# Performance work log

Hardware: AMD Instinct MI355X
Metric: run time of the kernel (lower is better)

## Reference

```python
import jax, jax.numpy as jnp
import numpy as np

B, S, HID = 1, 2048, 2048
H, KV, D = 32, 8, 64          # query heads, kv heads, head_dim
N_REP = H // KV
BASE = 10000.0


def rotate_half(x):
    x1, x2 = x[..., : D // 2], x[..., D // 2 :]
    return jnp.concatenate((-x2, x1), axis=-1)


def setup_inputs() -> dict:
    key = jax.random.key(0)
    ks = jax.random.split(key, 6)
    std = 0.02
    return {
        "hidden_states": jax.random.normal(ks[0], (B, S, HID), jnp.float32),
        "position_ids": jnp.broadcast_to(jnp.arange(S, dtype=jnp.int32), (B, S)),
        "powers": jax.random.normal(ks[1], (D // 2,), jnp.float32),
        "Wq": jax.random.normal(ks[2], (H * D, HID), jnp.float32) * std,
        "Wk": jax.random.normal(ks[3], (KV * D, HID), jnp.float32) * std,
        "Wv": jax.random.normal(ks[4], (KV * D, HID), jnp.float32) * std,
        "Wo": jax.random.normal(ks[5], (HID, H * D), jnp.float32) * std,
    }


def reference(hidden_states, position_ids, powers, Wq, Wk, Wv, Wo):
    bsz, q_len, _ = hidden_states.shape

    # QKV projections (no bias)
    q = (hidden_states @ Wq.T).reshape(bsz, q_len, H, D).transpose(0, 2, 1, 3)   # [B,H,S,D]
    k = (hidden_states @ Wk.T).reshape(bsz, q_len, KV, D).transpose(0, 2, 1, 3)  # [B,KV,S,D]
    v = (hidden_states @ Wv.T).reshape(bsz, q_len, KV, D).transpose(0, 2, 1, 3)

    # Learnable RoPE: inv_freq = base ** (-sigmoid(powers))
    inv_freq = 1.0 / (BASE ** jax.nn.sigmoid(powers))                 # [D/2]
    freqs = position_ids.astype(jnp.float32)[:, :, None] * inv_freq  # [B,S,D/2]
    emb = jnp.concatenate((freqs, freqs), axis=-1)                   # [B,S,D]
    cos = jnp.cos(emb)[:, None, :, :]                                # [B,1,S,D]
    sin = jnp.sin(emb)[:, None, :, :]

    q = q * cos + rotate_half(q) * sin
    k = k * cos + rotate_half(k) * sin

    # GQA: repeat_interleave kv heads
    k = jnp.repeat(k, N_REP, axis=1)  # [B,H,S,D]
    v = jnp.repeat(v, N_REP, axis=1)

    scores = jnp.einsum("bhqd,bhkd->bhqk", q, k) / np.sqrt(D).astype(np.float32)
    # additive causal mask (module is_causal=True)
    pos = jnp.arange(q_len)
    causal = jnp.where(pos[:, None] >= pos[None, :], 0.0, jnp.finfo(jnp.float32).min)
    scores = scores + causal

    probs = jax.nn.softmax(scores.astype(jnp.float32), axis=-1).astype(q.dtype)
    attn = jnp.einsum("bhqk,bhkd->bhqd", probs, v)                   # [B,H,S,D]
    attn = attn.transpose(0, 2, 1, 3).reshape(bsz, q_len, H * D)
    return attn @ Wo.T
```

## Files before the change

kernel.cpp:

```cpp
#include <hip/hip_runtime.h>

typedef unsigned short u16;
typedef __attribute__((ext_vector_type(8))) short short8;
typedef __attribute__((ext_vector_type(4))) short s16x4;
typedef __attribute__((ext_vector_type(4))) float f32x4;
typedef __attribute__((ext_vector_type(16))) float f32x16;
typedef __attribute__((ext_vector_type(4))) unsigned u32x4;

#define S_LEN 2048
#define HID 2048
#define NQH 32
#define NKV 8
#define HD 64
#define QKVN 3072
#define SCLOG2 0.1803368801111204f

__device__ __forceinline__ short f2b(float f){
  unsigned u = __builtin_bit_cast(unsigned, f);
  u += 0x7fffu + ((u >> 16) & 1u);
  return (short)(u >> 16);
}
__device__ __forceinline__ float b2f(u16 v){
  unsigned u = ((unsigned)v) << 16;
  return __builtin_bit_cast(float, u);
}
__device__ __forceinline__ void gll16(const void* g, void* l){
  __builtin_amdgcn_global_load_lds((const __attribute__((address_space(1))) void*)g,
                                   (__attribute__((address_space(3))) void*)l, 16, 0, 0);
}
__device__ __forceinline__ unsigned cvtpk(float a, float b){
  unsigned r;
  asm("v_cvt_pk_bf16_f32 %0, %1, %2" : "=v"(r) : "v"(a), "v"(b));
  return r;
}
__device__ __forceinline__ void pswap(unsigned &a, unsigned &b){
  asm volatile("v_permlane32_swap_b32 %0, %1" : "+v"(a), "+v"(b));
}
__device__ __forceinline__ float ex2(float x){
  float r; asm("v_exp_f32 %0, %1" : "=v"(r) : "v"(x)); return r;
}

__global__ __launch_bounds__(256) void cvt_all(const float* __restrict__ s0,
                                               const float* __restrict__ s1,
                                               const float* __restrict__ s2,
                                               const float* __restrict__ s3,
                                               const float* __restrict__ s4,
                                               u16* __restrict__ d0, u16* __restrict__ d1,
                                               u16* __restrict__ d2, u16* __restrict__ d3,
                                               u16* __restrict__ d4,
                                               const int* __restrict__ pos,
                                               const float* __restrict__ powers,
                                               float* __restrict__ cost,
                                               float* __restrict__ sint){
  int i = blockIdx.x * 256 + threadIdx.x;
  if (i >= 1835008) {
    int j = i - 1835008;
    int s = j >> 5, d = j & 31;
    float p = (float)pos[s];
    float w = powers[d];
    float sig = 1.0f / (1.0f + expf(-w));
    float inv = powf(10000.0f, -sig);
    float f = p * inv;
    cost[j] = cosf(f);
    sint[j] = sinf(f);
    return;
  }
  const float* s; u16* d; int off;
  if      (i <  524288){ s = s0; d = d0; off = i; }
  else if (i < 1048576){ s = s1; d = d1; off = i -  524288; }
  else if (i < 1179648){ s = s2; d = d2; off = i - 1048576; }
  else if (i < 1310720){ s = s3; d = d3; off = i - 1179648; }
  else                 { s = s4; d = d4; off = i - 1310720; }
  const float4* s4p = (const float4*)s;
  float4 a = s4p[off*2], b = s4p[off*2+1];
  short8 o = { f2b(a.x), f2b(a.y), f2b(a.z), f2b(a.w),
               f2b(b.x), f2b(b.y), f2b(b.z), f2b(b.w) };
  *(short8*)(d + (size_t)off*8) = o;
}

template<int MODE>
__global__ __launch_bounds__(256) void gemm_bt(const u16* __restrict__ A,
                                               const u16* __restrict__ B0,
                                               const u16* __restrict__ B1,
                                               const u16* __restrict__ B2,
                                               int n1, int n2,
                                               void* __restrict__ Cout,
                                               u16* __restrict__ vtOut,
                                               int M, int Ntot, int K,
                                               const float* __restrict__ cost,
                                               const float* __restrict__ sint){
  __shared__ alignas(16) u16 sA[2][64*64];
  __shared__ alignas(16) u16 sB[2][128*64];
  const int tid = threadIdx.x, lane = tid & 63, wv = tid >> 6;
  const int wr = wv >> 1, wc = wv & 1;
  const int m0 = blockIdx.y * 64, n0 = blockIdx.x * 128;
  const int lr = lane & 15, lg = lane >> 4;

  const u16* B;
  if (n0 < n1)      B = B0 + (size_t)n0 * K;
  else if (n0 < n2) B = B1 + (size_t)(n0 - n1) * K;
  else              B = B2 + (size_t)(n0 - n2) * K;

  const int sRow = tid >> 3;
  const int sCol = ((tid & 7) ^ (sRow & 7)) * 8;
  const u16* Arow = A + (size_t)(m0 + sRow)*K + sCol;
  const u16* Brow = B + (size_t)sRow*K + sCol;

  f32x4 acc[2][4] = {};
  const int NT = K >> 6;

  #pragma unroll
  for (int i = 0; i < 2; ++i)
    gll16(Arow + (size_t)i*32*K, (char*)&sA[0][0] + i*4096 + tid*16);
  #pragma unroll
  for (int i = 0; i < 4; ++i)
    gll16(Brow + (size_t)i*32*K, (char*)&sB[0][0] + i*4096 + tid*16);
  __syncthreads();

  for (int t = 0; t < NT; ++t) {
    const int cur = t & 1;
    if (t + 1 < NT) {
      const int kn = (t + 1) << 6;
      #pragma unroll
      for (int i = 0; i < 2; ++i)
        gll16(Arow + (size_t)i*32*K + kn, (char*)&sA[cur^1][0] + i*4096 + tid*16);
      #pragma unroll
      for (int i = 0; i < 4; ++i)
        gll16(Brow + (size_t)i*32*K + kn, (char*)&sB[cur^1][0] + i*4096 + tid*16);
    }
    const char* bA = (const char*)&sA[cur][0];
    const char* bB = (const char*)&sB[cur][0];
    #pragma unroll
    for (int kk = 0; kk < 64; kk += 32) {
      short8 af[2], bfr[4];
      #pragma unroll
      for (int m = 0; m < 2; ++m)
        af[m] = *(const short8*)(bA + (wr*32 + m*16 + lr)*128 + ((((kk>>3) + lg) ^ (lr & 7)) << 4));
      #pragma unroll
      for (int n = 0; n < 4; ++n)
        bfr[n] = *(const short8*)(bB + (wc*64 + n*16 + lr)*128 + ((((kk>>3) + lg) ^ (lr & 7)) << 4));
      #pragma unroll
      for (int m = 0; m < 2; ++m)
        #pragma unroll
        for (int n = 0; n < 4; ++n)
          acc[m][n] = __builtin_amdgcn_mfma_f32_16x16x32_bf16(af[m], bfr[n], acc[m][n], 0, 0, 0);
    }
    asm volatile("s_waitcnt vmcnt(0)" ::: "memory");
    __builtin_amdgcn_s_barrier();
  }

  if (MODE == 0 && n0 >= 2560) {
    #pragma unroll
    for (int n = 0; n < 4; ++n) {
      const int colv = n0 - 2560 + wc*64 + n*16 + lr;
      #pragma unroll
      for (int m = 0; m < 2; ++m) {
        const int row = m0 + wr*32 + m*16 + lg*4;
        s16x4 o = { f2b(acc[m][n][0]), f2b(acc[m][n][1]),
                    f2b(acc[m][n][2]), f2b(acc[m][n][3]) };
        *(s16x4*)&vtOut[(size_t)colv*S_LEN + row] = o;
      }
    }
  } else if (MODE == 0) {
    const float qsc = (n0 < n1) ? SCLOG2 : 1.0f;
    #pragma unroll
    for (int m = 0; m < 2; ++m)
      #pragma unroll
      for (int r = 0; r < 4; ++r) {
        int row = m0 + wr*32 + m*16 + lg*4 + r;
        float c0 = cost[row*32 + lr],      s0 = sint[row*32 + lr];
        float c1 = cost[row*32 + 16 + lr], s1 = sint[row*32 + 16 + lr];
        float x0 = acc[m][0][r], x1 = acc[m][1][r];
        float x2 = acc[m][2][r], x3 = acc[m][3][r];
        float o0 = (x0*c0 - x2*s0)*qsc, o2 = (x2*c0 + x0*s0)*qsc;
        float o1 = (x1*c1 - x3*s1)*qsc, o3 = (x3*c1 + x1*s1)*qsc;
        u16* cp = (u16*)Cout + (size_t)row*Ntot + n0 + wc*64 + lr;
        cp[0]  = (u16)f2b(o0);
        cp[16] = (u16)f2b(o1);
        cp[32] = (u16)f2b(o2);
        cp[48] = (u16)f2b(o3);
      }
  } else {
    #pragma unroll
    for (int m = 0; m < 2; ++m)
      #pragma unroll
      for (int n = 0; n < 4; ++n)
        #pragma unroll
        for (int r = 0; r < 4; ++r) {
          int row = m0 + wr*32 + m*16 + lg*4 + r;
          int col = n0 + wc*64 + n*16 + lr;
          ((float*)Cout)[(size_t)row*Ntot + col] = acc[m][n][r];
        }
  }
}

__global__ __launch_bounds__(256) void flash_attn(const u16* __restrict__ qkv,
                                                  const u16* __restrict__ vt,
                                                  u16* __restrict__ attn,
                                                  float* __restrict__ pO,
                                                  float* __restrict__ pL){
  __shared__ alignas(16) u16 sK[4][32*64];
  __shared__ alignas(16) u16 sVT[4][64*32];
  static const int c_tab[24] = {7,15,15,14,14,6,13,13,12,12,5,11,11,
                                10,10,4,9,9,8,8,3,2,1,0};
  static const int s_tab[24] = {2,0,1,0,1,2,0,1,0,1,2,0,1,
                                0,1,2,0,1,0,1,2,2,2,2};
  const int tid = threadIdx.x, lane = tid & 63, w = tid >> 6;
  const int h = blockIdx.x, kvh = h >> 2;
  const int chunk = c_tab[blockIdx.y];
  const int sl = s_tab[blockIdx.y];
  int t0, ntb;
  if (sl == 2) { t0 = 0; ntb = 4*chunk + 4; }
  else         { t0 = sl*2*(chunk + 1); ntb = 2*(chunk + 1); }

  const int l5 = lane & 31, hi = lane >> 5;
  const int q0w = chunk*128 + w*32;
  const int qg = q0w + l5;

  const int kRow = lane >> 3;
  const u16* srcK = qkv + (size_t)(8*w + kRow)*QKVN + HID + kvh*HD
                    + ((lane & 7) ^ (kRow & 7))*8;
  const int vRow = lane >> 2;
  const u16* srcV = vt + (size_t)(kvh*HD + 16*w + vRow)*S_LEN
                    + ((lane & 3) ^ (vRow & 3))*8;

  auto STAGE = [&](int t, int buf){
    gll16(srcK + (size_t)(t*32)*QKVN, (char*)&sK[buf][0]  + w*1024);
    gll16(srcV + t*32,                (char*)&sVT[buf][0] + w*1024);
  };

  short8 qf[4];
  #pragma unroll
  for (int cc = 0; cc < 4; ++cc)
    qf[cc] = *(const short8*)&qkv[(size_t)(q0w + l5)*QKVN + h*HD + cc*16 + hi*8];

  f32x16 accO[2] = {};
  float l_part = 0.f;

  STAGE(t0, 0);
  STAGE(t0 + 1, 1);

  auto QK = [&](const char* bK)->f32x16{
    short8 kf[4];
    #pragma unroll
    for (int cc = 0; cc < 4; ++cc)
      kf[cc] = *(const short8*)(bK + l5*128 + (((cc*2 + hi) ^ (l5 & 7))*16));
    __builtin_amdgcn_s_setprio(1);
    f32x16 za = {}, zb = {};
    za = __builtin_amdgcn_mfma_f32_32x32x16_bf16(kf[0], qf[0], za, 0, 0, 0);
    zb = __builtin_amdgcn_mfma_f32_32x32x16_bf16(kf[1], qf[1], zb, 0, 0, 0);
    za = __builtin_amdgcn_mfma_f32_32x32x16_bf16(kf[2], qf[2], za, 0, 0, 0);
    zb = __builtin_amdgcn_mfma_f32_32x32x16_bf16(kf[3], qf[3], zb, 0, 0, 0);
    __builtin_amdgcn_s_setprio(0);
    return za + zb;
  };

  auto SMPV = [&](int kt, const char* bV, f32x16& z){
    if (kt + 31 > q0w) {
      #pragma unroll
      for (int r = 0; r < 16; ++r) {
        const int k = kt + (r&3) + 8*(r>>2) + 4*hi;
        float e = ex2(z[r]);
        z[r] = (k > qg) ? 0.f : e;
      }
    } else {
      #pragma unroll
      for (int r = 0; r < 16; ++r) z[r] = ex2(z[r]);
    }
    float s0 = (z[0]+z[1]) + (z[2]+z[3]);
    float s1 = (z[4]+z[5]) + (z[6]+z[7]);
    float s2 = (z[8]+z[9]) + (z[10]+z[11]);
    float s3 = (z[12]+z[13]) + (z[14]+z[15]);
    l_part += (s0+s1) + (s2+s3);

    short8 pa[2];
    {
      unsigned a0 = cvtpk(z[0],  z[1]);
      unsigned c0 = cvtpk(z[2],  z[3]);
      unsigned b0 = cvtpk(z[4],  z[5]);
      unsigned d0 = cvtpk(z[6],  z[7]);
      pswap(a0, b0); pswap(c0, d0);
      u32x4 w0 = {a0, c0, b0, d0};
      pa[0] = __builtin_bit_cast(short8, w0);
      unsigned a1 = cvtpk(z[8],  z[9]);
      unsigned c1 = cvtpk(z[10], z[11]);
      unsigned b1 = cvtpk(z[12], z[13]);
      unsigned d1 = cvtpk(z[14], z[15]);
      pswap(a1, b1); pswap(c1, d1);
      u32x4 w1 = {a1, c1, b1, d1};
      pa[1] = __builtin_bit_cast(short8, w1);
    }
    __builtin_amdgcn_s_setprio(1);
    #pragma unroll
    for (int s4 = 0; s4 < 2; ++s4)
      #pragma unroll
      for (int db = 0; db < 2; ++db) {
        short8 vf = *(const short8*)(bV + (db*32 + l5)*64 + (((s4*2 + hi) ^ (l5 & 3))*16));
        accO[db] = __builtin_amdgcn_mfma_f32_32x32x16_bf16(vf, pa[s4], accO[db], 0, 0, 0);
      }
    __builtin_amdgcn_s_setprio(0);
  };

  for (int lt = 0; lt < ntb; lt += 2) {
    asm volatile("s_waitcnt vmcnt(0)" ::: "memory");
    __builtin_amdgcn_s_barrier();
    if (lt + 2 < ntb) STAGE(t0 + lt + 2, (lt + 2) & 3);
    if (lt + 3 < ntb) STAGE(t0 + lt + 3, (lt + 3) & 3);

    const int ktA = (t0 + lt)*32, ktB = ktA + 32;
    const bool doA = (ktA <= q0w + 31);
    const bool doB = (lt + 1 < ntb) && (ktB <= q0w + 31);
    const char* bKA = (const char*)&sK[lt & 3][0];
    const char* bVA = (const char*)&sVT[lt & 3][0];
    const char* bKB = (const char*)&sK[(lt + 1) & 3][0];
    const char* bVB = (const char*)&sVT[(lt + 1) & 3][0];

    f32x16 stA, stB;
    if (doA) stA = QK(bKA);
    if (doB) stB = QK(bKB);
    if (doA) SMPV(ktA, bVA, stA);
    if (doB) SMPV(ktB, bVB, stB);
  }

  const float l_run = l_part + __shfl_xor(l_part, 32);
  if (sl == 2) {
    const float invl = 1.0f / l_run;
    #pragma unroll
    for (int db = 0; db < 2; ++db)
      #pragma unroll
      for (int g2 = 0; g2 < 4; ++g2) {
        s16x4 o = { f2b(accO[db][g2*4+0]*invl), f2b(accO[db][g2*4+1]*invl),
                    f2b(accO[db][g2*4+2]*invl), f2b(accO[db][g2*4+3]*invl) };
        *(s16x4*)&attn[(size_t)(q0w + l5)*HID + h*HD + db*32 + g2*8 + hi*4] = o;
      }
  } else {
    const int slot = (h*8 + (chunk - 8))*2 + sl;
    const int row = w*32 + l5;
    float* po = pO + (size_t)slot*128*64 + (size_t)row*64;
    #pragma unroll
    for (int db = 0; db < 2; ++db)
      #pragma unroll
      for (int g2 = 0; g2 < 4; ++g2) {
        f32x4 v = { accO[db][g2*4+0], accO[db][g2*4+1],
                    accO[db][g2*4+2], accO[db][g2*4+3] };
        *(f32x4*)&po[db*32 + g2*8 + hi*4] = v;
      }
    if (lane < 32)
      pL[(size_t)slot*128 + row] = l_run;
  }
}

__global__ __launch_bounds__(256) void combine(const float* __restrict__ pO,
                                               const float* __restrict__ pL,
                                               u16* __restrict__ attn){
  int i = blockIdx.x * 256 + threadIdx.x;
  int d8 = i & 7;
  int row = (i >> 3) & 127;
  int cc = (i >> 10) & 7;
  int h = i >> 13;
  int slot0 = (h*8 + cc)*2;
  float l = pL[(size_t)slot0*128 + row] + pL[(size_t)(slot0+1)*128 + row];
  const float* p0 = pO + (size_t)slot0*128*64 + (size_t)row*64 + d8*8;
  const float* p1 = p0 + 128*64;
  const float inv = 1.0f / l;
  short8 o;
  #pragma unroll
  for (int j = 0; j < 8; ++j)
    o[j] = f2b((p0[j] + p1[j]) * inv);
  const int q = (8 + cc)*128 + row;
  *(short8*)&attn[(size_t)q*HID + h*HD + d8*8] = o;
}

extern "C" void kernel_launch(void* const* d_in, const int* in_sizes, int n_in,
                              void* d_out, int out_size, void* d_ws, size_t ws_size,
                              hipStream_t stream){
  const float* hs     = (const float*)d_in[0];
  const int*   pos    = (const int*)d_in[1];
  const float* powers = (const float*)d_in[2];
  const float* Wq     = (const float*)d_in[3];
  const float* Wk     = (const float*)d_in[4];
  const float* Wv     = (const float*)d_in[5];
  const float* Wo     = (const float*)d_in[6];
  float* out = (float*)d_out;

  char* ws = (char*)d_ws;
  auto take = [&](size_t bytes){ void* p = ws; ws += (bytes + 255) & ~(size_t)255; return p; };
  u16* hs_b  = (u16*)take((size_t)S_LEN*HID*2);
  u16* wq_b  = (u16*)take((size_t)HID*HID*2);
  u16* wk_b  = (u16*)take((size_t)NKV*HD*HID*2);
  u16* wv_b  = (u16*)take((size_t)NKV*HD*HID*2);
  u16* wo_b  = (u16*)take((size_t)HID*HID*2);
  u16* qkv   = (u16*)take((size_t)S_LEN*QKVN*2);
  u16* vt    = (u16*)take((size_t)NKV*HD*S_LEN*2);
  u16* attnb = (u16*)take((size_t)S_LEN*HID*2);
  float* cost = (float*)take((size_t)S_LEN*32*4);
  float* sint = (float*)take((size_t)S_LEN*32*4);
  float* pO   = (float*)take((size_t)NQH*8*2*128*64*4);
  float* pL   = (float*)take((size_t)NQH*8*2*128*4);

  cvt_all<<<7424, 256, 0, stream>>>(hs, Wq, Wk, Wv, Wo,
                                    hs_b, wq_b, wk_b, wv_b, wo_b,
                                    pos, powers, cost, sint);

  gemm_bt<0><<<dim3(QKVN/128, S_LEN/64), 256, 0, stream>>>(
      hs_b, wq_b, wk_b, wv_b, HID, HID + NKV*HD, qkv, vt,
      S_LEN, QKVN, HID, cost, sint);

  flash_attn<<<dim3(NQH, 24), 256, 0, stream>>>(qkv, vt, attnb, pO, pL);
  combine<<<1024, 256, 0, stream>>>(pO, pL, attnb);

  gemm_bt<1><<<dim3(HID/128, S_LEN/64), 256, 0, stream>>>(
      attnb, wo_b, wo_b, wo_b, 1<<28, 1<<29, out, nullptr,
      S_LEN, HID, HID, nullptr, nullptr);
}
```

Measured before the change: 116.3 us.

## Rebalance causal attention split-K into finer tables and store partials in bf16

Replaces the 24-block-per-head split scheme with a 40-entry table that splits query chunks 4..15 into 2-4 KV slices of at most 16 tiles each, so work per block is more uniform and more blocks run. The combine kernel now sums a variable number of partial slices per chunk. Partial outputs are stored as bf16 instead of fp32 to halve the partial write/read traffic, at some accuracy cost for unnormalized accumulators.

After: 117.7 us. No clear change (+1.2%).

```diff
diff --git a/kernel.cpp b/kernel.cpp
--- a/kernel.cpp
+++ b/kernel.cpp
@@ -197,21 +197,28 @@
 __global__ __launch_bounds__(256) void flash_attn(const u16* __restrict__ qkv,
                                                   const u16* __restrict__ vt,
                                                   u16* __restrict__ attn,
-                                                  float* __restrict__ pO,
+                                                  u16* __restrict__ pO,
                                                   float* __restrict__ pL){
   __shared__ alignas(16) u16 sK[4][32*64];
   __shared__ alignas(16) u16 sVT[4][64*32];
-  static const int c_tab[24] = {7,15,15,14,14,6,13,13,12,12,5,11,11,
-                                10,10,4,9,9,8,8,3,2,1,0};
-  static const int s_tab[24] = {2,0,1,0,1,2,0,1,0,1,2,0,1,
-                                0,1,2,0,1,0,1,2,2,2,2};
+  static const short c_tab[40]  = {15,15,15,15,14,14,11,11,11,10, 7, 7, 3,
+                                   14,14,13,13,13,13,12,12,10,10, 9, 9, 6, 6,
+                                   12,12, 9, 8, 8, 8, 5, 5, 2,  4, 4, 1, 0};
+  static const short t0_tab[40] = { 0,16,32,48, 0,16, 0,16,32, 0, 0,16, 0,
+                                   32,46, 0,14,28,42, 0,14,16,30, 0,14, 0,14,
+                                   28,40,28, 0,12,24, 0,12, 0,  0,10, 0, 0};
+  static const short nt_tab[40] = {16,16,16,16,16,16,16,16,16,16,16,16,16,
+                                   14,14,14,14,14,14,14,14,14,14,14,14,14,14,
+                                   12,12,12,12,12,12,12,12,12, 10,10, 8, 4};
+  static const short slot_tab[40]={32,33,34,35,28,29,17,18,19,14, 6, 7,-1,
+                                   30,31,24,25,26,27,20,21,15,16,11,12, 4, 5,
+                                   22,23,13, 8, 9,10, 2, 3,-1,  0, 1,-1,-1};
   const int tid = threadIdx.x, lane = tid & 63, w = tid >> 6;
   const int h = blockIdx.x, kvh = h >> 2;
   const int chunk = c_tab[blockIdx.y];
-  const int sl = s_tab[blockIdx.y];
-  int t0, ntb;
-  if (sl == 2) { t0 = 0; ntb = 4*chunk + 4; }
-  else         { t0 = sl*2*(chunk + 1); ntb = 2*(chunk + 1); }
+  const int t0 = t0_tab[blockIdx.y];
+  const int ntb = nt_tab[blockIdx.y];
+  const int slot = slot_tab[blockIdx.y];
 
   const int l5 = lane & 31, hi = lane >> 5;
   const int q0w = chunk*128 + w*32;
@@ -323,7 +330,7 @@
   }
 
   const float l_run = l_part + __shfl_xor(l_part, 32);
-  if (sl == 2) {
+  if (slot < 0) {
     const float invl = 1.0f / l_run;
     #pragma unroll
     for (int db = 0; db < 2; ++db)
@@ -334,40 +341,48 @@
         *(s16x4*)&attn[(size_t)(q0w + l5)*HID + h*HD + db*32 + g2*8 + hi*4] = o;
       }
   } else {
-    const int slot = (h*8 + (chunk - 8))*2 + sl;
+    const int gs = h*36 + slot;
     const int row = w*32 + l5;
-    float* po = pO + (size_t)slot*128*64 + (size_t)row*64;
+    u16* po = pO + (size_t)gs*128*64 + (size_t)row*64;
     #pragma unroll
     for (int db = 0; db < 2; ++db)
       #pragma unroll
       for (int g2 = 0; g2 < 4; ++g2) {
-        f32x4 v = { accO[db][g2*4+0], accO[db][g2*4+1],
-                    accO[db][g2*4+2], accO[db][g2*4+3] };
-        *(f32x4*)&po[db*32 + g2*8 + hi*4] = v;
+        s16x4 o = { f2b(accO[db][g2*4+0]), f2b(accO[db][g2*4+1]),
+                    f2b(accO[db][g2*4+2]), f2b(accO[db][g2*4+3]) };
+        *(s16x4*)&po[db*32 + g2*8 + hi*4] = o;
       }
     if (lane < 32)
-      pL[(size_t)slot*128 + row] = l_run;
-  }
-}
-
-__global__ __launch_bounds__(256) void combine(const float* __restrict__ pO,
+      pL[(size_t)gs*128 + row] = l_run;
+  }
+}
+
+__global__ __launch_bounds__(256) void combine(const u16* __restrict__ pO,
                                                const float* __restrict__ pL,
                                                u16* __restrict__ attn){
+  static const int base_tab[12] = {0,2,4,6,8,11,14,17,20,24,28,32};
+  static const int ns_tab[12]   = {2,2,2,2,3,3,3,3,4,4,4,4};
   int i = blockIdx.x * 256 + threadIdx.x;
   int d8 = i & 7;
   int row = (i >> 3) & 127;
-  int cc = (i >> 10) & 7;
-  int h = i >> 13;
-  int slot0 = (h*8 + cc)*2;
-  float l = pL[(size_t)slot0*128 + row] + pL[(size_t)(slot0+1)*128 + row];
-  const float* p0 = pO + (size_t)slot0*128*64 + (size_t)row*64 + d8*8;
-  const float* p1 = p0 + 128*64;
+  int cm = i >> 10;
+  int c4 = cm % 12;
+  int h = cm / 12;
+  const int ns = ns_tab[c4];
+  const int gs0 = h*36 + base_tab[c4];
+  float l = 0.f;
+  float acc[8] = {};
+  for (int s = 0; s < ns; ++s) {
+    const int gs = gs0 + s;
+    l += pL[(size_t)gs*128 + row];
+    short8 v = *(const short8*)&pO[((size_t)gs*128 + row)*64 + d8*8];
+    #pragma unroll
+    for (int j = 0; j < 8; ++j) acc[j] += b2f((u16)v[j]);
+  }
   const float inv = 1.0f / l;
-  short8 o;
-  #pragma unroll
-  for (int j = 0; j < 8; ++j)
-    o[j] = f2b((p0[j] + p1[j]) * inv);
-  const int q = (8 + cc)*128 + row;
+  short8 o = { f2b(acc[0]*inv), f2b(acc[1]*inv), f2b(acc[2]*inv), f2b(acc[3]*inv),
+               f2b(acc[4]*inv), f2b(acc[5]*inv), f2b(acc[6]*inv), f2b(acc[7]*inv) };
+  const int q = (4 + c4)*128 + row;
   *(short8*)&attn[(size_t)q*HID + h*HD + d8*8] = o;
 }
 
@@ -395,8 +410,8 @@
   u16* attnb = (u16*)take((size_t)S_LEN*HID*2);
   float* cost = (float*)take((size_t)S_LEN*32*4);
   float* sint = (float*)take((size_t)S_LEN*32*4);
-  float* pO   = (float*)take((size_t)NQH*8*2*128*64*4);
-  float* pL   = (float*)take((size_t)NQH*8*2*128*4);
+  u16* pO    = (u16*)take((size_t)NQH*36*128*64*2);
+  float* pL  = (float*)take((size_t)NQH*36*128*4);
 
   cvt_all<<<7424, 256, 0, stream>>>(hs, Wq, Wk, Wv, Wo,
                                     hs_b, wq_b, wk_b, wv_b, wo_b,
@@ -406,8 +421,8 @@
       hs_b, wq_b, wk_b, wv_b, HID, HID + NKV*HD, qkv, vt,
       S_LEN, QKVN, HID, cost, sint);
 
-  flash_attn<<<dim3(NQH, 24), 256, 0, stream>>>(qkv, vt, attnb, pO, pL);
-  combine<<<1024, 256, 0, stream>>>(pO, pL, attnb);
+  flash_attn<<<dim3(NQH, 40), 256, 0, stream>>>(qkv, vt, attnb, pO, pL);
+  combine<<<1536, 256, 0, stream>>>(pO, pL, attnb);
 
   gemm_bt<1><<<dim3(HID/128, S_LEN/64), 256, 0, stream>>>(
       attnb, wo_b, wo_b, wo_b, 1<<28, 1<<29, out, nullptr,
```
